# Kernel optimization log

Hardware: AMD Instinct MI355X
Metric: run time of the kernel (lower is better)

Reference implementation:

```python
import jax, jax.numpy as jnp
import numpy as np

B, T, V, WD = 32, 2048, 50000, 300        # batch, max_doc_len, batch vocab, word_dim
P, L, ND = 150, 7, 2                      # total patterns, max_pattern_length, num_diags
BIAS_SCALE = 1.0
ZERO = -100.0                             # max-plus semiring zero (repo: neg_infinity = -100*ones)
# end state per pattern = pattern_length - 1, for pattern_specs {5:50, 6:50, 7:50}
END_STATES = np.concatenate([np.full(50, 4), np.full(50, 5), np.full(50, 6)]).astype(np.int32)


def setup_inputs() -> dict:
    key = jax.random.key(0)
    ks = jax.random.split(key, 10)
    diags = jax.random.normal(ks[0], (P * ND * L, WD), jnp.float32)
    diags = diags / jnp.linalg.norm(diags, axis=1, keepdims=True)  # normalize() in __init__
    return {
        "embeddings_matrix": jax.random.normal(ks[1], (WD, V), jnp.float32),
        "diags": diags,
        "bias": jax.random.normal(ks[2], (P * ND * L, 1), jnp.float32),
        "epsilon": jax.random.normal(ks[3], (P, L - 1), jnp.float32),
        "mlp_w0": jax.random.normal(ks[4], (P, 100), jnp.float32) * 0.1,
        "mlp_b0": jnp.zeros((100,), jnp.float32),
        "mlp_w1": jax.random.normal(ks[5], (100, 2), jnp.float32) * 0.1,
        "mlp_b1": jnp.zeros((2,), jnp.float32),
        "docs": jax.random.randint(ks[6], (B, T), 0, V),
        "doc_lens": jax.random.randint(ks[7], (B,), 5, T + 1),
    }


def reference(embeddings_matrix, diags, bias, epsilon, mlp_w0, mlp_b0, mlp_w1, mlp_b1, docs, doc_lens):
    # Max-plus semiring: from_float = identity, times = +, plus = max, one = 0, zero = -100.
    # Transition scores for every token in the batch vocabulary: [V, P*ND*L]
    trans = (diags @ embeddings_matrix + BIAS_SCALE * bias).T
    # Gather per doc token, reshape, time-major: [T, B, P, ND, L]
    tm = trans[docs].reshape(B, T, P, ND, L).transpose(1, 0, 2, 3, 4)

    end_states = jnp.asarray(END_STATES)               # [P]
    active = jnp.arange(T)[:, None] < doc_lens[None, :]  # [T, B]

    zero_pad = jnp.full((B, P, 1), ZERO, trans.dtype)
    restart_pad = jnp.zeros((B, P, 1), trans.dtype)      # semiring one
    hid0 = jnp.full((B, P, L), ZERO, trans.dtype).at[:, :, 0].set(0.0)
    scores0 = jnp.full((B, P), ZERO, trans.dtype)
    eps_val = epsilon                                    # epsilon_scale = semiring one (=0) -> identity

    def step(carry, xs):
        hid, sc = carry
        tmat, act = xs  # tmat: [B, P, ND, L], act: [B]
        # epsilon transitions (shift by one state, additive in max-plus)
        after_eps = jnp.maximum(hid, jnp.concatenate([zero_pad, hid[:, :, :-1] + eps_val], axis=2))
        # main-path transitions (diag index -1), with restart padding at state 0
        main = jnp.concatenate([restart_pad, after_eps[:, :, :-1] + tmat[:, :, -1, :-1]], axis=2)
        # self loops (diag index 0); self_loop_scale = semiring one = 0
        self_loop = hid + tmat[:, :, 0, :]
        hid = jnp.maximum(main, self_loop)
        end_vals = jnp.take_along_axis(hid, end_states[None, :, None], axis=2)[:, :, 0]  # [B, P]
        sc = jnp.where(act[:, None], jnp.maximum(sc, end_vals), sc)
        return (hid, sc), None

    (_, scores), _ = jax.lax.scan(step, (hid0, scores0), (tm, active))
    # MLP head: Linear -> relu -> Linear
    h = scores @ mlp_w0 + mlp_b0
    return jax.nn.relu(h) @ mlp_w1 + mlp_b1
```

## Files before the change

kernel.cpp:

```cpp
#include <hip/hip_runtime.h>
#include <stdint.h>

#define B_   32
#define T_   2048
#define V_   50000
#define WD_  300
#define P_   150
#define KP   320
#define MP   2112
#define MB2  2176
#define NPAD2 50176
#define VT_  391
#define MT_  17
#define NWG3 6664
#define NEGC (-1.0e30f)

#define WS_DIAGSB      32112640u
#define WS_TRANS_BIG   54067200u
#define WS_TRANS_SMALL 33505280u
#define WS_AUX_BIG     265267200u
#define WS_AUX_SMALL   244705280u
#define AUX_BYTES      864260u
#define WS_NEED_BIG    (WS_AUX_BIG + AUX_BYTES)
#define WS_NEED_SMALL  (WS_AUX_SMALL + AUX_BYTES)

typedef __attribute__((ext_vector_type(8))) short bf16x8;
typedef __attribute__((ext_vector_type(4))) float f32x4;

#define GLOAD_LDS16(gp, lp) __builtin_amdgcn_global_load_lds( \
    (__attribute__((address_space(1))) void*)(gp), \
    (__attribute__((address_space(3))) void*)(lp), 16, 0, 0)

__device__ __forceinline__ unsigned short f2bf(float f){
  unsigned u = __builtin_bit_cast(unsigned, f);
  u = u + 0x7fffu + ((u >> 16) & 1u);
  return (unsigned short)(u >> 16);
}
__device__ __forceinline__ float bf_lo(unsigned u){ return __builtin_bit_cast(float, u << 16); }
__device__ __forceinline__ float bf_hi(unsigned u){ return __builtin_bit_cast(float, u & 0xffff0000u); }

__global__ __launch_bounds__(256) void k_transpose_emb(const float* __restrict__ emb,
                                                       unsigned short* __restrict__ embT){
  __shared__ float tile[32][65];
  int v0 = blockIdx.x * 64, k0 = blockIdx.y * 32;
  int tid = threadIdx.x;
  #pragma unroll
  for (int it = 0; it < 8; ++it){
    int idx = it * 256 + tid;
    int kk = idx >> 6, vv = idx & 63;
    int k = k0 + kk, v = v0 + vv;
    float val = 0.f;
    if (k < WD_ && v < V_) val = emb[(size_t)k * V_ + v];
    tile[kk][vv] = val;
  }
  __syncthreads();
  int row = tid >> 2, c = tid & 3;
  unsigned short e[8];
  #pragma unroll
  for (int i = 0; i < 8; ++i) e[i] = f2bf(tile[c*8 + i][row]);
  uint4 pk;
  pk.x = (unsigned)e[0] | ((unsigned)e[1] << 16);
  pk.y = (unsigned)e[2] | ((unsigned)e[3] << 16);
  pk.z = (unsigned)e[4] | ((unsigned)e[5] << 16);
  pk.w = (unsigned)e[6] | ((unsigned)e[7] << 16);
  *(uint4*)&embT[(size_t)(v0 + row) * KP + k0 + c*8] = pk;
}

__global__ __launch_bounds__(256) void k_conv_diags(const float* __restrict__ diags,
                                                    unsigned short* __restrict__ diagsB){
  int gid = blockIdx.x * 256 + threadIdx.x;
  int m = gid / 80;
  int k4 = (gid % 80) * 4;
  unsigned short e[4];
  #pragma unroll
  for (int i = 0; i < 4; ++i){
    int k = k4 + i;
    float v = (m < 2100 && k < WD_) ? diags[m * WD_ + k] : 0.f;
    e[i] = f2bf(v);
  }
  uint2 pk;
  pk.x = (unsigned)e[0] | ((unsigned)e[1] << 16);
  pk.y = (unsigned)e[2] | ((unsigned)e[3] << 16);
  *(uint2*)&diagsB[(size_t)m * KP + k4] = pk;
}

__global__ __launch_bounds__(256) void k_zero(int* __restrict__ used, int* __restrict__ counter){
  int i = blockIdx.x * 256 + threadIdx.x;
  if (i < NPAD2) used[i] = 0;
  if (i == 0) *counter = 0;
}
__global__ __launch_bounds__(256) void k_mark(const int* __restrict__ docs,
                                              const int* __restrict__ dlens,
                                              int* __restrict__ used){
  int i = blockIdx.x * 256 + threadIdx.x;
  int b = i >> 11, t = i & 2047;
  if (t < dlens[b]) used[docs[i]] = 1;
}
__global__ __launch_bounds__(256) void k_compact(const int* __restrict__ used,
                                                 int* __restrict__ remap,
                                                 int* __restrict__ inv,
                                                 int* __restrict__ counter){
  int v = blockIdx.x * 256 + threadIdx.x;
  if (v >= V_) return;
  if (used[v]){
    int id = atomicAdd(counter, 1);
    remap[v] = id;
    inv[id] = v;
  }
}
__global__ __launch_bounds__(256) void k_docsC(const int* __restrict__ docs,
                                               const int* __restrict__ dlens,
                                               const int* __restrict__ remap,
                                               int* __restrict__ docsC){
  int i = blockIdx.x * 256 + threadIdx.x;
  int b = i >> 11, t = i & 2047;
  docsC[i] = (t < dlens[b]) ? remap[docs[i]] : 0;
}

__global__ __launch_bounds__(256, 4) void k_gemm(const unsigned short* __restrict__ embT,
                                                 const unsigned short* __restrict__ diagsB,
                                                 const float* __restrict__ bias,
                                                 const int* __restrict__ inv,
                                                 const int* __restrict__ nusedp,
                                                 unsigned short* __restrict__ trans){
  __shared__ char smem[33792];
  int nused = *nusedp;
  int orig = blockIdx.x;
  int xcd = orig & 7, idx0 = orig >> 3;
  int vt = (idx0 / MT_) * 8 + xcd;
  int mt = idx0 % MT_;
  int v0 = vt * 128, m0 = mt * 128;
  if (v0 >= nused) return;

  int tid = threadIdx.x;
  int w = tid >> 6, l = tid & 63;
  int wv = w & 1, wm = w >> 1;
  int lrow = l & 15, lq = l >> 4;

  int rA0 = tid >> 2, rA1 = 64 + (tid >> 2);
  size_t ga0 = (size_t)((v0 + rA0 < nused) ? inv[v0 + rA0] : 0) * KP;
  size_t ga1 = (size_t)((v0 + rA1 < nused) ? inv[v0 + rA1] : 0) * KP;

  f32x4 acc[4][4];
  #pragma unroll
  for (int i = 0; i < 4; ++i)
    #pragma unroll
    for (int j = 0; j < 4; ++j)
      acc[i][j] = (f32x4){0.f, 0.f, 0.f, 0.f};

  auto STAGE = [&](int buf, int kt){
    int k0 = kt * 32;
    char* bA = smem + buf * 16384;
    char* bB = bA + 8192;
    int slot = tid & 3;
    {
      int idx = tid;
      int sc = slot ^ ((rA0 >> 1) & 3);
      GLOAD_LDS16(&embT[ga0 + k0 + sc * 8], bA + idx * 16);
      int row = idx >> 2;
      int scB = slot ^ ((row >> 1) & 3);
      GLOAD_LDS16(&diagsB[(size_t)(m0 + row) * KP + k0 + scB * 8], bB + idx * 16);
    }
    {
      int idx = 256 + tid;
      int sc = slot ^ ((rA1 >> 1) & 3);
      GLOAD_LDS16(&embT[ga1 + k0 + sc * 8], bA + idx * 16);
      int row = idx >> 2;
      int scB = slot ^ ((row >> 1) & 3);
      GLOAD_LDS16(&diagsB[(size_t)(m0 + row) * KP + k0 + scB * 8], bB + idx * 16);
    }
  };

  STAGE(0, 0);
  #pragma unroll
  for (int kt = 0; kt < 10; ++kt){
    if (kt < 9){
      STAGE((kt + 1) & 1, kt + 1);
      asm volatile("s_waitcnt vmcnt(4)" ::: "memory");
    } else {
      asm volatile("s_waitcnt vmcnt(0)" ::: "memory");
    }
    __builtin_amdgcn_s_barrier();
    __builtin_amdgcn_sched_barrier(0);
    char* bA = smem + (kt & 1) * 16384;
    char* bB = bA + 8192;
    bf16x8 af[4], bg[4];
    #pragma unroll
    for (int i = 0; i < 4; ++i){
      int row = wv * 64 + i * 16 + lrow;
      af[i] = *(const bf16x8*)(bA + row * 64 + (lq ^ ((row >> 1) & 3)) * 16);
    }
    #pragma unroll
    for (int j = 0; j < 4; ++j){
      int row = wm * 64 + j * 16 + lrow;
      bg[j] = *(const bf16x8*)(bB + row * 64 + (lq ^ ((row >> 1) & 3)) * 16);
    }
    #pragma unroll
    for (int i = 0; i < 4; ++i)
      #pragma unroll
      for (int j = 0; j < 4; ++j)
        acc[i][j] = __builtin_amdgcn_mfma_f32_16x16x32_bf16(af[i], bg[j], acc[i][j], 0, 0, 0);
    __builtin_amdgcn_sched_barrier(0);
    __builtin_amdgcn_s_barrier();
  }

  float bv4[4];
  #pragma unroll
  for (int j = 0; j < 4; ++j){
    int mg = m0 + wm * 64 + j * 16 + lrow;
    bv4[j] = (mg < 2100) ? bias[mg] : 0.f;
  }
  unsigned short* eb = (unsigned short*)smem;
  #pragma unroll
  for (int i = 0; i < 4; ++i)
    #pragma unroll
    for (int j = 0; j < 4; ++j)
      #pragma unroll
      for (int r = 0; r < 4; ++r){
        int row = wv * 64 + i * 16 + lq * 4 + r;
        int col = wm * 64 + j * 16 + lrow;
        eb[row * 132 + col] = f2bf(acc[i][j][r] + bv4[j]);
      }
  __syncthreads();
  #pragma unroll
  for (int it = 0; it < 16; ++it){
    int idx2 = it * 256 + tid;
    int row = idx2 >> 5, chq = idx2 & 31;
    int vg = v0 + row, mg = m0 + chq * 4;
    if (vg < nused && mg < MP){
      uint2 val = *(const uint2*)(smem + row * 264 + chq * 8);
      *(uint2*)&trans[(size_t)vg * MP + mg] = val;
    }
  }
}

template<int CH>
__global__ __launch_bounds__(192) void k_scan(const unsigned short* __restrict__ trans,
                                              const int* __restrict__ docsC,
                                              const int* __restrict__ doc_lens,
                                              const float* __restrict__ epsilon,
                                              float* __restrict__ chunkout){
  constexpr int NCHT = T_ / CH;
  constexpr int NG = CH / 2;
  __shared__ int sdocs[CH];
  __shared__ char rows[2][2][3][1792];
  int b = blockIdx.x / NCHT, ch = blockIdx.x % NCHT;
  int doclen = doc_lens[b];
  int tbase = ch * CH;
  if (tbase >= doclen) return;
  int tid = threadIdx.x;
  if (tid < CH) sdocs[tid] = docsC[b * T_ + tbase + tid];
  __syncthreads();

  int w = tid >> 6, l = tid & 63;
  int p = tid;
  bool act_p = p < P_;
  float eps_r[6] = {0,0,0,0,0,0};
  int endsel = 0;
  if (act_p){
    #pragma unroll
    for (int i = 0; i < 6; ++i) eps_r[i] = epsilon[p*6 + i];
    endsel = p / 50;
  }

  float col[7][7], bvec[7], uvec[7], wmax;
  #pragma unroll
  for (int j = 0; j < 7; ++j)
    #pragma unroll
    for (int l2 = 0; l2 < 7; ++l2) col[j][l2] = (j == l2) ? 0.f : NEGC;
  #pragma unroll
  for (int l2 = 0; l2 < 7; ++l2){ bvec[l2] = NEGC; uvec[l2] = NEGC; }
  wmax = NEGC;

  const char* transB = (const char*)trans;
  int sliceOff = 1792 * w;
  bool part0 = (w < 2) ? true : (l < 40);
  bool part1 = (w < 2) && (l < 48);

  uint4 rg[2][2];
  #pragma unroll
  for (int r = 0; r < 2; ++r){ rg[r][0] = make_uint4(0,0,0,0); rg[r][1] = make_uint4(0,0,0,0); }

  auto LOADG = [&](int g){
    #pragma unroll
    for (int r = 0; r < 2; ++r){
      const char* src = transB + (size_t)sdocs[g*2 + r] * (MP*2) + sliceOff;
      if (part0) rg[r][0] = *(const uint4*)(src + l * 16);
      if (part1) rg[r][1] = *(const uint4*)(src + (64 + l) * 16);
    }
  };
  auto WRITEG = [&](int buf){
    #pragma unroll
    for (int r = 0; r < 2; ++r){
      char* dst = rows[buf][r][w];
      if (part0) *(uint4*)(dst + l * 16) = rg[r][0];
      if (part1) *(uint4*)(dst + (64 + l) * 16) = rg[r][1];
    }
  };

  auto stepL = [&](const char* rp, bool act){
    unsigned q[7];
    #pragma unroll
    for (int i = 0; i < 7; ++i) q[i] = *(const unsigned*)(rp + 4*i);
    float tsf[7], tmn[6];
    tsf[0]=bf_lo(q[0]); tsf[1]=bf_hi(q[0]);
    tsf[2]=bf_lo(q[1]); tsf[3]=bf_hi(q[1]);
    tsf[4]=bf_lo(q[2]); tsf[5]=bf_hi(q[2]);
    tsf[6]=bf_lo(q[3]); tmn[0]=bf_hi(q[3]);
    tmn[1]=bf_lo(q[4]); tmn[2]=bf_hi(q[4]);
    tmn[3]=bf_lo(q[5]); tmn[4]=bf_hi(q[5]);
    tmn[5]=bf_lo(q[6]);
    #pragma unroll
    for (int j = 0; j < 7; ++j){
      #pragma unroll
      for (int l2 = 6; l2 >= 1; --l2){
        if (l2 < j) continue;
        if (l2 == j){ col[j][l2] = col[j][l2] + tsf[l2]; continue; }
        float ae;
        if (l2 - 1 == j) ae = col[j][l2-1];
        else ae = fmaxf(col[j][l2-1], col[j][l2-2] + eps_r[l2-2]);
        col[j][l2] = fmaxf(ae + tmn[l2-1], col[j][l2] + tsf[l2]);
      }
      if (j == 0) col[0][0] += tsf[0];
    }
    #pragma unroll
    for (int l2 = 6; l2 >= 1; --l2){
      float ae;
      if (l2 == 1) ae = fmaxf(bvec[0], -100.0f);
      else ae = fmaxf(bvec[l2-1], bvec[l2-2] + eps_r[l2-2]);
      bvec[l2] = fmaxf(ae + tmn[l2-1], bvec[l2] + tsf[l2]);
    }
    bvec[0] = fmaxf(0.0f, bvec[0] + tsf[0]);
    if (act){
      #pragma unroll
      for (int j = 0; j < 7; ++j){
        float c4 = (j <= 4) ? col[j][4] : NEGC;
        float c5 = (j <= 5) ? col[j][5] : NEGC;
        float c6 = col[j][6];
        float ce = (endsel == 0) ? c4 : ((endsel == 1) ? c5 : c6);
        uvec[j] = fmaxf(uvec[j], ce);
      }
      float be = (endsel == 0) ? bvec[4] : ((endsel == 1) ? bvec[5] : bvec[6]);
      wmax = fmaxf(wmax, be);
    }
  };

  LOADG(0);
  WRITEG(0);
  for (int g = 0; g < NG; ++g){
    if (g + 1 < NG) LOADG(g + 1);
    if (act_p){
      stepL(&rows[g & 1][0][w][l * 28], (tbase + g*2)     < doclen);
      stepL(&rows[g & 1][1][w][l * 28], (tbase + g*2 + 1) < doclen);
    }
    if (g + 1 < NG) WRITEG((g + 1) & 1);
  }

  if (act_p){
    float out[44];
    int idx = 0;
    #pragma unroll
    for (int j = 0; j < 7; ++j)
      #pragma unroll
      for (int l2 = j; l2 < 7; ++l2) out[idx++] = col[j][l2];
    #pragma unroll
    for (int l2 = 0; l2 < 7; ++l2) out[28 + l2] = bvec[l2];
    #pragma unroll
    for (int l2 = 0; l2 < 7; ++l2) out[35 + l2] = uvec[l2];
    out[42] = wmax; out[43] = 0.f;
    float* dst = chunkout + ((size_t)(b * NCHT + ch) * P_ + p) * 44;
    #pragma unroll
    for (int i = 0; i < 11; ++i){
      float4 t2 = make_float4(out[4*i], out[4*i+1], out[4*i+2], out[4*i+3]);
      ((float4*)dst)[i] = t2;
    }
  }
}

__global__ __launch_bounds__(192) void k_combine_mlp(const float* __restrict__ chunkout,
                                                     const int* __restrict__ doc_lens,
                                                     const float* __restrict__ w0,
                                                     const float* __restrict__ b0,
                                                     const float* __restrict__ w1,
                                                     const float* __restrict__ b1,
                                                     float* __restrict__ out,
                                                     int nch, int chsz){
  __shared__ float ssc[P_];
  __shared__ float sh[100];
  int b = blockIdx.x, tid = threadIdx.x;
  if (tid < P_){
    int p = tid;
    int doclen = doc_lens[b];
    int nact = (doclen + chsz - 1) / chsz;
    if (nact > nch) nact = nch;
    float h[7] = {0.f, -100.f, -100.f, -100.f, -100.f, -100.f, -100.f};
    float sc = -100.f;
    for (int ch = 0; ch < nact; ++ch){
      const float* rec = chunkout + ((size_t)(b * nch + ch) * P_ + p) * 44;
      float r[44];
      #pragma unroll
      for (int i = 0; i < 11; ++i){
        float4 t = ((const float4*)rec)[i];
        r[4*i] = t.x; r[4*i+1] = t.y; r[4*i+2] = t.z; r[4*i+3] = t.w;
      }
      #pragma unroll
      for (int j = 0; j < 7; ++j) sc = fmaxf(sc, r[35 + j] + h[j]);
      sc = fmaxf(sc, r[42]);
      constexpr int off[7] = {0, 7, 13, 18, 22, 25, 27};
      float nh[7];
      #pragma unroll
      for (int l = 0; l < 7; ++l){
        float v = r[28 + l];
        #pragma unroll
        for (int j = 0; j < 7; ++j){
          if (j <= l) v = fmaxf(v, r[off[j] + (l - j)] + h[j]);
        }
        nh[l] = v;
      }
      #pragma unroll
      for (int l = 0; l < 7; ++l) h[l] = nh[l];
    }
    ssc[p] = sc;
  }
  __syncthreads();
  if (tid < 100){
    float a = b0[tid];
    for (int pp = 0; pp < P_; ++pp) a += ssc[pp] * w0[pp * 100 + tid];
    sh[tid] = fmaxf(a, 0.f);
  }
  __syncthreads();
  if (tid < 2){
    float o = b1[tid];
    for (int j = 0; j < 100; ++j) o += sh[j] * w1[j * 2 + tid];
    out[b * 2 + tid] = o;
  }
}

extern "C" void kernel_launch(void* const* d_in, const int* in_sizes, int n_in,
                              void* d_out, int out_size, void* d_ws, size_t ws_size,
                              hipStream_t stream){
  const float* emb   = (const float*)d_in[0];
  const float* diags = (const float*)d_in[1];
  const float* bias  = (const float*)d_in[2];
  const float* eps   = (const float*)d_in[3];
  const float* w0    = (const float*)d_in[4];
  const float* b0    = (const float*)d_in[5];
  const float* w1    = (const float*)d_in[6];
  const float* b1    = (const float*)d_in[7];
  const int* docs    = (const int*)d_in[8];
  const int* dlens   = (const int*)d_in[9];

  if (ws_size < (size_t)WS_NEED_SMALL) return;
  bool big = ws_size >= (size_t)WS_NEED_BIG;

  char* ws = (char*)d_ws;
  unsigned short* embT   = (unsigned short*)(ws);
  unsigned short* diagsB = (unsigned short*)(ws + WS_DIAGSB);
  unsigned short* trans  = (unsigned short*)(ws + (big ? WS_TRANS_BIG : WS_TRANS_SMALL));
  char* aux              = ws + (big ? WS_AUX_BIG : WS_AUX_SMALL);
  int* used    = (int*)(aux);
  int* remap   = (int*)(aux + 200704u);
  int* inv     = (int*)(aux + 401408u);
  int* docsC   = (int*)(aux + 602112u);
  int* counter = (int*)(aux + 864256u);
  float* chunkout = (float*)(ws);
  float* outp = (float*)d_out;

  k_transpose_emb<<<dim3(NPAD2/64, KP/32), 256, 0, stream>>>(emb, embT);
  k_conv_diags<<<(MB2*80 + 255)/256, 256, 0, stream>>>(diags, diagsB);
  k_zero<<<NPAD2/256, 256, 0, stream>>>(used, counter);
  k_mark<<<B_*T_/256, 256, 0, stream>>>(docs, dlens, used);
  k_compact<<<(V_ + 255)/256, 256, 0, stream>>>(used, remap, inv, counter);
  k_docsC<<<B_*T_/256, 256, 0, stream>>>(docs, dlens, remap, docsC);
  k_gemm<<<NWG3, 256, 0, stream>>>(embT, diagsB, bias, inv, counter, trans);
  if (big){
    k_scan<32><<<B_ * 64, 192, 0, stream>>>(trans, docsC, dlens, eps, chunkout);
    k_combine_mlp<<<B_, 192, 0, stream>>>(chunkout, dlens, w0, b0, w1, b1, outp, 64, 32);
  } else {
    k_scan<64><<<B_ * 32, 192, 0, stream>>>(trans, docsC, dlens, eps, chunkout);
    k_combine_mlp<<<B_, 192, 0, stream>>>(chunkout, dlens, w0, b0, w1, b1, outp, 32, 64);
  }
}
```

Baseline: 188.6 us.

## Replace register-staged double buffer with direct global-to-LDS ring prefetch in scan

The scan kernel now streams each timestep's transition row slice straight into a six-slot shared-memory ring using direct global-to-LDS loads, keeping five steps in flight and waiting on explicit vmcnt counts. This replaces the earlier scheme that loaded two steps into registers and then copied them to a double-buffered LDS array. The aim is to hide gather latency for the serial recurrence and drop the register-to-LDS copy. It depends on each wave reading only the slots it wrote itself, since there is no barrier, and it relies on the hand-counted vmcnt thresholds being correct. The full unroll over CH also grows code size.

```diff
diff --git a/kernel.cpp b/kernel.cpp
--- a/kernel.cpp
+++ b/kernel.cpp
@@ -241,9 +241,8 @@
                                               const float* __restrict__ epsilon,
                                               float* __restrict__ chunkout){
   constexpr int NCHT = T_ / CH;
-  constexpr int NG = CH / 2;
   __shared__ int sdocs[CH];
-  __shared__ char rows[2][2][3][1792];
+  __shared__ unsigned ringU[3 * 6 * 512];
   int b = blockIdx.x / NCHT, ch = blockIdx.x % NCHT;
   int doclen = doc_lens[b];
   int tbase = ch * CH;
@@ -274,34 +273,18 @@
 
   const char* transB = (const char*)trans;
   int sliceOff = 1792 * w;
-  bool part0 = (w < 2) ? true : (l < 40);
-  bool part1 = (w < 2) && (l < 48);
-
-  uint4 rg[2][2];
-  #pragma unroll
-  for (int r = 0; r < 2; ++r){ rg[r][0] = make_uint4(0,0,0,0); rg[r][1] = make_uint4(0,0,0,0); }
-
-  auto LOADG = [&](int g){
-    #pragma unroll
-    for (int r = 0; r < 2; ++r){
-      const char* src = transB + (size_t)sdocs[g*2 + r] * (MP*2) + sliceOff;
-      if (part0) rg[r][0] = *(const uint4*)(src + l * 16);
-      if (part1) rg[r][1] = *(const uint4*)(src + (64 + l) * 16);
-    }
+
+  auto STAGE = [&](int s, int slot){
+    const char* src = transB + (size_t)sdocs[s] * (MP*2) + sliceOff;
+    char* dst = (char*)&ringU[(w * 6 + slot) * 512];
+    GLOAD_LDS16(src + l * 16, dst);
+    GLOAD_LDS16(src + 1024 + l * 16, dst + 1024);
   };
-  auto WRITEG = [&](int buf){
-    #pragma unroll
-    for (int r = 0; r < 2; ++r){
-      char* dst = rows[buf][r][w];
-      if (part0) *(uint4*)(dst + l * 16) = rg[r][0];
-      if (part1) *(uint4*)(dst + (64 + l) * 16) = rg[r][1];
-    }
-  };
-
-  auto stepL = [&](const char* rp, bool act){
+
+  auto stepL = [&](int base, bool act){
     unsigned q[7];
     #pragma unroll
-    for (int i = 0; i < 7; ++i) q[i] = *(const unsigned*)(rp + 4*i);
+    for (int i = 0; i < 7; ++i) q[i] = ringU[base + i];
     float tsf[7], tmn[6];
     tsf[0]=bf_lo(q[0]); tsf[1]=bf_hi(q[0]);
     tsf[2]=bf_lo(q[1]); tsf[3]=bf_hi(q[1]);
@@ -345,15 +328,17 @@
     }
   };
 
-  LOADG(0);
-  WRITEG(0);
-  for (int g = 0; g < NG; ++g){
-    if (g + 1 < NG) LOADG(g + 1);
-    if (act_p){
-      stepL(&rows[g & 1][0][w][l * 28], (tbase + g*2)     < doclen);
-      stepL(&rows[g & 1][1][w][l * 28], (tbase + g*2 + 1) < doclen);
-    }
-    if (g + 1 < NG) WRITEG((g + 1) & 1);
+  STAGE(0, 0); STAGE(1, 1); STAGE(2, 2); STAGE(3, 3); STAGE(4, 4);
+  #pragma unroll
+  for (int s = 0; s < CH; ++s){
+    int rem = CH - 1 - s;
+    if      (rem >= 4) asm volatile("s_waitcnt vmcnt(8)" ::: "memory");
+    else if (rem == 3) asm volatile("s_waitcnt vmcnt(6)" ::: "memory");
+    else if (rem == 2) asm volatile("s_waitcnt vmcnt(4)" ::: "memory");
+    else if (rem == 1) asm volatile("s_waitcnt vmcnt(2)" ::: "memory");
+    else               asm volatile("s_waitcnt vmcnt(0)" ::: "memory");
+    if (act_p) stepL((w * 6 + (s % 6)) * 512 + l * 7, (tbase + s) < doclen);
+    if (s + 5 < CH) STAGE(s + 5, (s + 5) % 6);
   }
 
   if (act_p){
```

Measured after the change: 205.2 us. 1.09x slower.
